# Optimization experiments

Hardware: AMD Instinct MI355X
Metric: run time of the kernel (lower is better)

Reference implementation:

```python
import jax, jax.numpy as jnp
import numpy as np

N_NODES = 50000
N_EDGES = 800000
D_IN = 128
D_HID = 128


def setup_inputs() -> dict:
    key = jax.random.key(0)
    ks = jax.random.split(key, 9)
    x = jax.random.normal(ks[0], (N_NODES, D_IN), dtype=jnp.float32)
    edge_index = jax.random.randint(ks[1], (2, N_EDGES), 0, N_NODES, dtype=jnp.int64)
    s = 1.0 / np.sqrt(D_IN)
    # SAGEConv params: lin_l acts on mean-aggregated neighbors (has bias),
    # lin_r acts on the root/self features (no bias). Stored as [in, out].
    Wl1 = jax.random.uniform(ks[2], (D_IN, D_HID), jnp.float32, -s, s)
    Wr1 = jax.random.uniform(ks[3], (D_IN, D_HID), jnp.float32, -s, s)
    b1 = jax.random.uniform(ks[4], (D_HID,), jnp.float32, -s, s)
    Wl2 = jax.random.uniform(ks[5], (D_HID, D_HID), jnp.float32, -s, s)
    Wr2 = jax.random.uniform(ks[6], (D_HID, D_HID), jnp.float32, -s, s)
    b2 = jax.random.uniform(ks[7], (D_HID,), jnp.float32, -s, s)
    return {"x": x, "edge_index": edge_index, "Wl1": Wl1, "Wr1": Wr1,
            "b1": b1, "Wl2": Wl2, "Wr2": Wr2, "b2": b2}


def _sage_conv(h, src, dst, n_nodes, Wl, Wr, b):
    # gather neighbor features, mean-aggregate at targets (PyG mean aggr)
    msg = h[src]  # [E, d]
    summed = jax.ops.segment_sum(msg, dst, num_segments=n_nodes)  # [N, d]
    cnt = jax.ops.segment_sum(jnp.ones((src.shape[0], 1), h.dtype), dst,
                              num_segments=n_nodes)  # [N, 1]
    agg = summed / jnp.maximum(cnt, 1.0)  # isolated nodes -> 0, matches scatter-mean
    return agg @ Wl + b + h @ Wr


def reference(x, edge_index, Wl1, Wr1, b1, Wl2, Wr2, b2):
    src = edge_index[0]  # source nodes j (messages flow j -> i)
    dst = edge_index[1]  # target nodes i
    n = x.shape[0]
    h = _sage_conv(x, src, dst, n, Wl1, Wr1, b1)
    h = jax.nn.relu(h)  # dropout is identity in eval mode
    out = _sage_conv(h, src, dst, n, Wl2, Wr2, b2)
    return out
```

## Files before the change

kernel.cpp:

```cpp
#include <hip/hip_runtime.h>
#include <hip/hip_bf16.h>

#define DD 128
#define BSH 8
#define CHUNK 4096
#define MM_STREAMS 1024

typedef __attribute__((ext_vector_type(8))) short short8v;
typedef __attribute__((ext_vector_type(4))) float f32x4;

static __device__ __forceinline__ ushort f2bf(float f) {
    __hip_bfloat16 b = __float2bfloat16(f);
    return *reinterpret_cast<ushort*>(&b);
}


__global__ __launch_bounds__(256) void k_hist(const int* __restrict__ ei,
                                              int* __restrict__ hist, int E, int NB) {
    __shared__ int lh[256];
    int t = threadIdx.x;
    lh[t] = 0;
    __syncthreads();
    int e0 = blockIdx.x * CHUNK;
    int e1 = min(e0 + CHUNK, E);
    for (int e = e0 + t; e < e1; e += 256)
        atomicAdd(&lh[ei[E + e] >> BSH], 1);
    __syncthreads();
    if (t < NB) hist[blockIdx.x * NB + t] = lh[t];
}

__global__ __launch_bounds__(1024) void k_hscan(int* __restrict__ hist,
                                                int* __restrict__ bbase,
                                                int nblk, int NB, int E) {
    __shared__ int part[4][256];
    __shared__ int s[256];
    int t = threadIdx.x;
    int b = t & 255, g = t >> 8;
    int q = (nblk + 3) >> 2;
    int lo = g * q, hi = min(lo + q, nblk);
    int sum = 0;
    if (b < NB)
        for (int blk = lo; blk < hi; ++blk) sum += hist[blk * NB + b];
    part[g][b] = sum;
    __syncthreads();
    if (g == 0) s[b] = part[0][b] + part[1][b] + part[2][b] + part[3][b];
    __syncthreads();
    for (int off = 1; off < 256; off <<= 1) {
        int v = 0;
        if (g == 0 && b >= off) v = s[b - off];
        __syncthreads();
        if (g == 0) s[b] += v;
        __syncthreads();
    }
    int base = (b == 0) ? 0 : s[b - 1];
    if (g == 0 && b < NB) bbase[b] = base;
    if (t == 0) bbase[NB] = E;
    int run = base;
    for (int gg = 0; gg < g; ++gg) run += part[gg][b];
    if (b < NB)
        for (int blk = lo; blk < hi; ++blk) {
            int tmp = hist[blk * NB + b];
            hist[blk * NB + b] = run;
            run += tmp;
        }
}

__global__ __launch_bounds__(256) void k_scatter(const int* __restrict__ ei,
                                                 const int* __restrict__ hist,
                                                 uint2* __restrict__ pairs, int E, int NB) {
    __shared__ int lofs[256];
    __shared__ int lh[256];
    int t = threadIdx.x;
    int blk = blockIdx.x;
    lh[t] = 0;
    if (t < NB) lofs[t] = hist[blk * NB + t];
    __syncthreads();
    int e0 = blk * CHUNK, e1 = min(e0 + CHUNK, E);
    for (int e = e0 + t; e < e1; e += 256) {
        int sN = ei[e];
        int d = ei[E + e];
        int b = d >> BSH;
        int lp = atomicAdd(&lh[b], 1);
        pairs[lofs[b] + lp] = make_uint2((uint)sN, (uint)d);
    }
}

__global__ __launch_bounds__(256) void k_csr(const uint2* __restrict__ pairs,
                                             const int* __restrict__ bbase,
                                             int* __restrict__ rowptr,
                                             int* __restrict__ eidx,
                                             int n, int E, int NB) {
    __shared__ int lc[256];
    __shared__ int cur[256];
    int t = threadIdx.x;
    int b = blockIdx.x;
    int node0 = b << BSH;
    lc[t] = 0;
    __syncthreads();
    int r0 = bbase[b], r1 = bbase[b + 1];
    for (int i = r0 + t; i < r1; i += 256)
        atomicAdd(&lc[(int)pairs[i].y - node0], 1);
    __syncthreads();
    int c0 = lc[t];
#pragma unroll
    for (int off = 1; off < 256; off <<= 1) {
        int u = (t >= off) ? lc[t - off] : 0;
        __syncthreads();
        lc[t] += u;
        __syncthreads();
    }
    int rp = r0 + lc[t] - c0;
    int node = node0 + t;
    if (node < n) rowptr[node] = rp;
    if (b == NB - 1 && t == 0) rowptr[n] = E;
    cur[t] = rp;
    __syncthreads();
    for (int i = r0 + t; i < r1; i += 256) {
        uint2 pr = pairs[i];
        int p = atomicAdd(&cur[(int)pr.y - node0], 1);
        eidx[p] = (int)pr.x;
    }
}


__global__ __launch_bounds__(256) void k_cast(const float* __restrict__ x,
                                              ushort* __restrict__ xbf, int n4) {
    int i = blockIdx.x * blockDim.x + threadIdx.x;
    if (i >= n4) return;
    float4 v = reinterpret_cast<const float4*>(x)[i];
    ushort4 o;
    o.x = f2bf(v.x); o.y = f2bf(v.y); o.z = f2bf(v.z); o.w = f2bf(v.w);
    reinterpret_cast<ushort4*>(xbf)[i] = o;
}


__global__ __launch_bounds__(256) void k_prepw(const float* __restrict__ Wl,
                                               const float* __restrict__ Wr,
                                               ushort* __restrict__ Wt) {
    int idx = blockIdx.x * 256 + threadIdx.x;
    int nn = idx >> 8, k = idx & 255;
    float v = (k < 128) ? Wl[k * 128 + nn] : Wr[(k - 128) * 128 + nn];
    Wt[nn * 256 + k] = f2bf(v);
}


#define ACC8(v)                                    \
    acc[0] += __uint_as_float((v).x << 16);        \
    acc[1] += __uint_as_float((v).x & 0xffff0000u);\
    acc[2] += __uint_as_float((v).y << 16);        \
    acc[3] += __uint_as_float((v).y & 0xffff0000u);\
    acc[4] += __uint_as_float((v).z << 16);        \
    acc[5] += __uint_as_float((v).z & 0xffff0000u);\
    acc[6] += __uint_as_float((v).w << 16);        \
    acc[7] += __uint_as_float((v).w & 0xffff0000u);

__global__ __launch_bounds__(256) void k_aggb(const ushort* __restrict__ hin,
                                              const int* __restrict__ rowptr,
                                              const int* __restrict__ eidx,
                                              ushort* __restrict__ aggout, int n) {
    int w = (int)((blockIdx.x * (unsigned)blockDim.x + threadIdx.x) >> 6);
    int lane = threadIdx.x & 63;
    if (w >= n) return;
    int eg = lane >> 4;
    int c16 = lane & 15;
    int beg = rowptr[w], end = rowptr[w + 1];
    const uint4* base = reinterpret_cast<const uint4*>(hin);

    float acc[8];
#pragma unroll
    for (int i = 0; i < 8; ++i) acc[i] = 0.f;

    int e = beg;
    for (; e + 16 <= end; e += 16) {
        int id[4];
        uint4 v[4];
#pragma unroll
        for (int j = 0; j < 4; ++j) id[j] = eidx[e + 4 * j + eg];
#pragma unroll
        for (int j = 0; j < 4; ++j) v[j] = base[(size_t)id[j] * 16 + c16];
#pragma unroll
        for (int j = 0; j < 4; ++j) { ACC8(v[j]); }
    }
    for (; e + 8 <= end; e += 8) {
        int i0 = eidx[e + eg];
        int i1 = eidx[e + 4 + eg];
        uint4 va = base[(size_t)i0 * 16 + c16];
        uint4 vb = base[(size_t)i1 * 16 + c16];
        ACC8(va);
        ACC8(vb);
    }
    for (; e < end; e += 4) {
        int ee = e + eg;
        if (ee < end) {
            int i0 = eidx[ee];
            uint4 va = base[(size_t)i0 * 16 + c16];
            ACC8(va);
        }
    }

#pragma unroll
    for (int i = 0; i < 8; ++i) {
        acc[i] += __shfl_xor(acc[i], 16);
        acc[i] += __shfl_xor(acc[i], 32);
    }

    if (eg == 0) {
        float inv = 1.0f / fmaxf((float)(end - beg), 1.0f);
        uint4 o;
        o.x = ((uint)f2bf(acc[1] * inv) << 16) | (uint)f2bf(acc[0] * inv);
        o.y = ((uint)f2bf(acc[3] * inv) << 16) | (uint)f2bf(acc[2] * inv);
        o.z = ((uint)f2bf(acc[5] * inv) << 16) | (uint)f2bf(acc[4] * inv);
        o.w = ((uint)f2bf(acc[7] * inv) << 16) | (uint)f2bf(acc[6] * inv);
        reinterpret_cast<uint4*>(aggout)[(size_t)w * 16 + c16] = o;
    }
}


__global__ __launch_bounds__(256, 8) void k_mm(const ushort* __restrict__ Alow,
                                               const ushort* __restrict__ Ahigh,
                                               const ushort* __restrict__ Wt,
                                               const float* __restrict__ bias,
                                               void* __restrict__ outp,
                                               int n, int ntiles, int relu, int outBf16) {
    int t = threadIdx.x;
    int wv = t >> 6;
    int l = t & 63;
    int lr = l & 15;
    int lk = l >> 4;
    int gw = blockIdx.x * 4 + wv;
    int nt = gw & 7;
    int stream = gw >> 3;

    short8v bf[8];
    const ushort* wbase = Wt + (size_t)(nt * 16 + lr) * 256 + lk * 8;
#pragma unroll
    for (int ks = 0; ks < 8; ++ks)
        bf[ks] = *reinterpret_cast<const short8v*>(wbase + ks * 32);

    int col = nt * 16 + lr;
    float bv = bias[col];

    for (int tile = stream; tile < ntiles; tile += MM_STREAMS) {
        int m0 = tile * 16;
        int arow = m0 + lr;
        if (arow >= n) arow = n - 1;
        const ushort* alo = Alow + (size_t)arow * DD + lk * 8;
        const ushort* ahi = Ahigh + (size_t)arow * DD + lk * 8;

        f32x4 acc = (f32x4){0.f, 0.f, 0.f, 0.f};
#pragma unroll
        for (int ks = 0; ks < 4; ++ks) {
            short8v af = *reinterpret_cast<const short8v*>(alo + ks * 32);
            acc = __builtin_amdgcn_mfma_f32_16x16x32_bf16(af, bf[ks], acc, 0, 0, 0);
        }
#pragma unroll
        for (int ks = 0; ks < 4; ++ks) {
            short8v af = *reinterpret_cast<const short8v*>(ahi + ks * 32);
            acc = __builtin_amdgcn_mfma_f32_16x16x32_bf16(af, bf[ks + 4], acc, 0, 0, 0);
        }

        int row0 = m0 + lk * 4;
#pragma unroll
        for (int r = 0; r < 4; ++r) {
            int row = row0 + r;
            if (row < n) {
                float v = acc[r] + bv;
                if (relu) v = fmaxf(v, 0.f);
                if (outBf16) {
                    reinterpret_cast<ushort*>(outp)[(size_t)row * DD + col] = f2bf(v);
                } else {
                    reinterpret_cast<float*>(outp)[(size_t)row * DD + col] = v;
                }
            }
        }
    }
}


extern "C" void kernel_launch(void* const* d_in, const int* in_sizes, int n_in,
                              void* d_out, int out_size, void* d_ws, size_t ws_size,
                              hipStream_t stream) {
    const float* x   = (const float*)d_in[0];
    const int*   ei  = (const int*)d_in[1];
    const float* Wl1 = (const float*)d_in[2];
    const float* Wr1 = (const float*)d_in[3];
    const float* b1  = (const float*)d_in[4];
    const float* Wl2 = (const float*)d_in[5];
    const float* Wr2 = (const float*)d_in[6];
    const float* b2  = (const float*)d_in[7];
    float* out = (float*)d_out;

    int n = in_sizes[0] / DD;
    int E = in_sizes[1] / 2;

    int NB   = (n + 255) >> 8;
    int nblk = (E + CHUNK - 1) / CHUNK;

    char* ws = (char*)d_ws;
    size_t off = 0;
    auto take = [&](size_t bytes) -> void* {
        void* p = ws + off;
        off = (off + bytes + 255) & ~(size_t)255;
        return p;
    };
    int* rowptr    = (int*)take(((size_t)n + 1) * 4);
    int* hist      = (int*)take((size_t)nblk * NB * 4);
    int* bbase     = (int*)take(((size_t)NB + 1) * 4);
    int* eidx      = (int*)take((size_t)E * 4);
    uint2* pairs   = (uint2*)take((size_t)E * 8);
    ushort* xbf    = (ushort*)take((size_t)n * DD * 2);
    ushort* hbf    = (ushort*)take((size_t)n * DD * 2);
    ushort* aggbf  = (ushort*)take((size_t)n * DD * 2);
    ushort* Wt1    = (ushort*)take((size_t)DD * 256 * 2);
    ushort* Wt2    = (ushort*)take((size_t)DD * 256 * 2);

    int ntiles = (n + 15) / 16;

    k_hist<<<nblk, 256, 0, stream>>>(ei, hist, E, NB);
    k_hscan<<<1, 1024, 0, stream>>>(hist, bbase, nblk, NB, E);
    k_scatter<<<nblk, 256, 0, stream>>>(ei, hist, pairs, E, NB);
    k_csr<<<NB, 256, 0, stream>>>(pairs, bbase, rowptr, eidx, n, E, NB);

    int n4 = n * DD / 4;
    k_cast<<<(n4 + 255) / 256, 256, 0, stream>>>(x, xbf, n4);
    k_prepw<<<128, 256, 0, stream>>>(Wl1, Wr1, Wt1);
    k_prepw<<<128, 256, 0, stream>>>(Wl2, Wr2, Wt2);

    int aggBlocks = (n + 3) / 4;
    int mmBlocks  = MM_STREAMS * 8 / 4;

    k_aggb<<<aggBlocks, 256, 0, stream>>>(xbf, rowptr, eidx, aggbf, n);
    k_mm<<<mmBlocks, 256, 0, stream>>>(aggbf, xbf, Wt1, b1, hbf, n, ntiles, 1, 1);
    k_aggb<<<aggBlocks, 256, 0, stream>>>(hbf, rowptr, eidx, aggbf, n);
    k_mm<<<mmBlocks, 256, 0, stream>>>(aggbf, hbf, Wt2, b2, out, n, ntiles, 0, 0);
}
```

Before: 186.9 us.

## Fuse prep kernels, compress edge indices to 16 bits, one node per quarter-wave

Merges the histogram, feature cast and weight-prep kernels into one launch to cut launch overhead. Packs CSR pairs into 32-bit words and stores neighbor indices as ushort to halve index traffic in the CSR build and the two aggregation passes. The aggregation kernel now gives each 16-lane group its own node instead of splitting one node's edges across four groups, which removes the cross-group shuffle reduction. Storing source indices in 16 bits truncates any node id of 65536 or more, which the node count allows for.

Result: faster. 182.5 us (-2.4%).

```diff
diff --git a/kernel.cpp b/kernel.cpp
--- a/kernel.cpp
+++ b/kernel.cpp
@@ -15,18 +15,52 @@
 }
 
 
-__global__ __launch_bounds__(256) void k_hist(const int* __restrict__ ei,
-                                              int* __restrict__ hist, int E, int NB) {
+__global__ __launch_bounds__(256) void k_prep(const int* __restrict__ ei,
+                                              int* __restrict__ hist, int E, int NB, int nblk,
+                                              const float* __restrict__ x,
+                                              ushort* __restrict__ xbf, int n4, int castBlocks,
+                                              const float* __restrict__ Wl1,
+                                              const float* __restrict__ Wr1,
+                                              ushort* __restrict__ Wt1,
+                                              const float* __restrict__ Wl2,
+                                              const float* __restrict__ Wr2,
+                                              ushort* __restrict__ Wt2) {
     __shared__ int lh[256];
     int t = threadIdx.x;
-    lh[t] = 0;
-    __syncthreads();
-    int e0 = blockIdx.x * CHUNK;
-    int e1 = min(e0 + CHUNK, E);
-    for (int e = e0 + t; e < e1; e += 256)
-        atomicAdd(&lh[ei[E + e] >> BSH], 1);
-    __syncthreads();
-    if (t < NB) hist[blockIdx.x * NB + t] = lh[t];
+    int b = blockIdx.x;
+
+    if (b < nblk) {
+        lh[t] = 0;
+        __syncthreads();
+        int e0 = b * CHUNK;
+        int e1 = min(e0 + CHUNK, E);
+        for (int e = e0 + t; e < e1; e += 256)
+            atomicAdd(&lh[ei[E + e] >> BSH], 1);
+        __syncthreads();
+        if (t < NB) hist[b * NB + t] = lh[t];
+        return;
+    }
+    b -= nblk;
+    if (b < castBlocks) {
+        int i = b * 256 + t;
+        if (i < n4) {
+            float4 v = reinterpret_cast<const float4*>(x)[i];
+            ushort4 o;
+            o.x = f2bf(v.x); o.y = f2bf(v.y); o.z = f2bf(v.z); o.w = f2bf(v.w);
+            reinterpret_cast<ushort4*>(xbf)[i] = o;
+        }
+        return;
+    }
+    b -= castBlocks;
+    {
+        const float* Wl = (b < 128) ? Wl1 : Wl2;
+        const float* Wr = (b < 128) ? Wr1 : Wr2;
+        ushort* Wt = (b < 128) ? Wt1 : Wt2;
+        int idx = (b & 127) * 256 + t;
+        int nn = idx >> 8, k = idx & 255;
+        float v = (k < 128) ? Wl[k * 128 + nn] : Wr[(k - 128) * 128 + nn];
+        Wt[nn * 256 + k] = f2bf(v);
+    }
 }
 
 __global__ __launch_bounds__(1024) void k_hscan(int* __restrict__ hist,
@@ -67,7 +101,7 @@
 
 __global__ __launch_bounds__(256) void k_scatter(const int* __restrict__ ei,
                                                  const int* __restrict__ hist,
-                                                 uint2* __restrict__ pairs, int E, int NB) {
+                                                 uint* __restrict__ pairs, int E, int NB) {
     __shared__ int lofs[256];
     __shared__ int lh[256];
     int t = threadIdx.x;
@@ -81,14 +115,14 @@
         int d = ei[E + e];
         int b = d >> BSH;
         int lp = atomicAdd(&lh[b], 1);
-        pairs[lofs[b] + lp] = make_uint2((uint)sN, (uint)d);
-    }
-}
-
-__global__ __launch_bounds__(256) void k_csr(const uint2* __restrict__ pairs,
+        pairs[lofs[b] + lp] = ((uint)(d & 255) << 16) | (uint)sN;
+    }
+}
+
+__global__ __launch_bounds__(256) void k_csr(const uint* __restrict__ pairs,
                                              const int* __restrict__ bbase,
                                              int* __restrict__ rowptr,
-                                             int* __restrict__ eidx,
+                                             ushort* __restrict__ eidx,
                                              int n, int E, int NB) {
     __shared__ int lc[256];
     __shared__ int cur[256];
@@ -99,7 +133,7 @@
     __syncthreads();
     int r0 = bbase[b], r1 = bbase[b + 1];
     for (int i = r0 + t; i < r1; i += 256)
-        atomicAdd(&lc[(int)pairs[i].y - node0], 1);
+        atomicAdd(&lc[pairs[i] >> 16], 1);
     __syncthreads();
     int c0 = lc[t];
 #pragma unroll
@@ -116,31 +150,10 @@
     cur[t] = rp;
     __syncthreads();
     for (int i = r0 + t; i < r1; i += 256) {
-        uint2 pr = pairs[i];
-        int p = atomicAdd(&cur[(int)pr.y - node0], 1);
-        eidx[p] = (int)pr.x;
-    }
-}
-
-
-__global__ __launch_bounds__(256) void k_cast(const float* __restrict__ x,
-                                              ushort* __restrict__ xbf, int n4) {
-    int i = blockIdx.x * blockDim.x + threadIdx.x;
-    if (i >= n4) return;
-    float4 v = reinterpret_cast<const float4*>(x)[i];
-    ushort4 o;
-    o.x = f2bf(v.x); o.y = f2bf(v.y); o.z = f2bf(v.z); o.w = f2bf(v.w);
-    reinterpret_cast<ushort4*>(xbf)[i] = o;
-}
-
-
-__global__ __launch_bounds__(256) void k_prepw(const float* __restrict__ Wl,
-                                               const float* __restrict__ Wr,
-                                               ushort* __restrict__ Wt) {
-    int idx = blockIdx.x * 256 + threadIdx.x;
-    int nn = idx >> 8, k = idx & 255;
-    float v = (k < 128) ? Wl[k * 128 + nn] : Wr[(k - 128) * 128 + nn];
-    Wt[nn * 256 + k] = f2bf(v);
+        uint pr = pairs[i];
+        int p = atomicAdd(&cur[pr >> 16], 1);
+        eidx[p] = (ushort)(pr & 0xFFFFu);
+    }
 }
 
 
@@ -156,63 +169,45 @@
 
 __global__ __launch_bounds__(256) void k_aggb(const ushort* __restrict__ hin,
                                               const int* __restrict__ rowptr,
-                                              const int* __restrict__ eidx,
+                                              const ushort* __restrict__ eidx,
                                               ushort* __restrict__ aggout, int n) {
-    int w = (int)((blockIdx.x * (unsigned)blockDim.x + threadIdx.x) >> 6);
+    int wave = (int)((blockIdx.x * (unsigned)blockDim.x + threadIdx.x) >> 6);
     int lane = threadIdx.x & 63;
-    if (w >= n) return;
-    int eg = lane >> 4;
+    int grp = lane >> 4;
     int c16 = lane & 15;
-    int beg = rowptr[w], end = rowptr[w + 1];
+    int node = wave * 4 + grp;
+    if (node >= n) return;
+
+    int beg = rowptr[node], end = rowptr[node + 1];
     const uint4* base = reinterpret_cast<const uint4*>(hin);
 
     float acc[8];
 #pragma unroll
     for (int i = 0; i < 8; ++i) acc[i] = 0.f;
 
-    int e = beg;
-    for (; e + 16 <= end; e += 16) {
-        int id[4];
-        uint4 v[4];
-#pragma unroll
-        for (int j = 0; j < 4; ++j) id[j] = eidx[e + 4 * j + eg];
-#pragma unroll
-        for (int j = 0; j < 4; ++j) v[j] = base[(size_t)id[j] * 16 + c16];
-#pragma unroll
-        for (int j = 0; j < 4; ++j) { ACC8(v[j]); }
-    }
-    for (; e + 8 <= end; e += 8) {
-        int i0 = eidx[e + eg];
-        int i1 = eidx[e + 4 + eg];
-        uint4 va = base[(size_t)i0 * 16 + c16];
-        uint4 vb = base[(size_t)i1 * 16 + c16];
-        ACC8(va);
-        ACC8(vb);
-    }
-    for (; e < end; e += 4) {
-        int ee = e + eg;
-        if (ee < end) {
-            int i0 = eidx[ee];
-            uint4 va = base[(size_t)i0 * 16 + c16];
-            ACC8(va);
-        }
-    }
-
-#pragma unroll
-    for (int i = 0; i < 8; ++i) {
-        acc[i] += __shfl_xor(acc[i], 16);
-        acc[i] += __shfl_xor(acc[i], 32);
-    }
-
-    if (eg == 0) {
-        float inv = 1.0f / fmaxf((float)(end - beg), 1.0f);
-        uint4 o;
-        o.x = ((uint)f2bf(acc[1] * inv) << 16) | (uint)f2bf(acc[0] * inv);
-        o.y = ((uint)f2bf(acc[3] * inv) << 16) | (uint)f2bf(acc[2] * inv);
-        o.z = ((uint)f2bf(acc[5] * inv) << 16) | (uint)f2bf(acc[4] * inv);
-        o.w = ((uint)f2bf(acc[7] * inv) << 16) | (uint)f2bf(acc[6] * inv);
-        reinterpret_cast<uint4*>(aggout)[(size_t)w * 16 + c16] = o;
-    }
+    for (int e = beg; e < end; e += 4) {
+        int m = end - e;
+        int i0 = eidx[e];
+        int i1 = eidx[e + (m > 1 ? 1 : 0)];
+        int i2 = eidx[e + (m > 2 ? 2 : 0)];
+        int i3 = eidx[e + (m > 3 ? 3 : 0)];
+        uint4 v0 = base[(size_t)i0 * 16 + c16];
+        uint4 v1 = base[(size_t)i1 * 16 + c16];
+        uint4 v2 = base[(size_t)i2 * 16 + c16];
+        uint4 v3 = base[(size_t)i3 * 16 + c16];
+        ACC8(v0);
+        if (m > 1) { ACC8(v1); }
+        if (m > 2) { ACC8(v2); }
+        if (m > 3) { ACC8(v3); }
+    }
+
+    float inv = 1.0f / fmaxf((float)(end - beg), 1.0f);
+    uint4 o;
+    o.x = ((uint)f2bf(acc[1] * inv) << 16) | (uint)f2bf(acc[0] * inv);
+    o.y = ((uint)f2bf(acc[3] * inv) << 16) | (uint)f2bf(acc[2] * inv);
+    o.z = ((uint)f2bf(acc[5] * inv) << 16) | (uint)f2bf(acc[4] * inv);
+    o.w = ((uint)f2bf(acc[7] * inv) << 16) | (uint)f2bf(acc[6] * inv);
+    reinterpret_cast<uint4*>(aggout)[(size_t)node * 16 + c16] = o;
 }
 
 
@@ -306,8 +301,8 @@
     int* rowptr    = (int*)take(((size_t)n + 1) * 4);
     int* hist      = (int*)take((size_t)nblk * NB * 4);
     int* bbase     = (int*)take(((size_t)NB + 1) * 4);
-    int* eidx      = (int*)take((size_t)E * 4);
-    uint2* pairs   = (uint2*)take((size_t)E * 8);
+    ushort* eidx   = (ushort*)take((size_t)E * 2 + 16);
+    uint* pairs    = (uint*)take((size_t)E * 4);
     ushort* xbf    = (ushort*)take((size_t)n * DD * 2);
     ushort* hbf    = (ushort*)take((size_t)n * DD * 2);
     ushort* aggbf  = (ushort*)take((size_t)n * DD * 2);
@@ -315,18 +310,18 @@
     ushort* Wt2    = (ushort*)take((size_t)DD * 256 * 2);
 
     int ntiles = (n + 15) / 16;
-
-    k_hist<<<nblk, 256, 0, stream>>>(ei, hist, E, NB);
+    int n4 = n * DD / 4;
+    int castBlocks = (n4 + 255) / 256;
+    int prepBlocks = nblk + castBlocks + 256;
+
+    k_prep<<<prepBlocks, 256, 0, stream>>>(ei, hist, E, NB, nblk,
+                                           x, xbf, n4, castBlocks,
+                                           Wl1, Wr1, Wt1, Wl2, Wr2, Wt2);
     k_hscan<<<1, 1024, 0, stream>>>(hist, bbase, nblk, NB, E);
     k_scatter<<<nblk, 256, 0, stream>>>(ei, hist, pairs, E, NB);
     k_csr<<<NB, 256, 0, stream>>>(pairs, bbase, rowptr, eidx, n, E, NB);
 
-    int n4 = n * DD / 4;
-    k_cast<<<(n4 + 255) / 256, 256, 0, stream>>>(x, xbf, n4);
-    k_prepw<<<128, 256, 0, stream>>>(Wl1, Wr1, Wt1);
-    k_prepw<<<128, 256, 0, stream>>>(Wl2, Wr2, Wt2);
-
-    int aggBlocks = (n + 3) / 4;
+    int aggBlocks = (n + 15) / 16;
     int mmBlocks  = MM_STREAMS * 8 / 4;
 
     k_aggb<<<aggBlocks, 256, 0, stream>>>(xbf, rowptr, eidx, aggbf, n);
```
